# Optimization experiments

Hardware: AMD Instinct MI355X
Metric: run time of the kernel (lower is better)

The kernel has to match this reference:

```python
import jax, jax.numpy as jnp
import numpy as np

B, F, DEPTH = 8192, 256, 6

def entmax15(x):
    # exact 1.5-entmax along the last axis (sort-based algorithm)
    x = x / 2.0
    x = x - jnp.max(x, axis=-1, keepdims=True)
    xs = -jnp.sort(-x, axis=-1)                      # descending sort
    d = x.shape[-1]
    rho = jnp.arange(1, d + 1, dtype=x.dtype)
    mean = jnp.cumsum(xs, axis=-1) / rho
    mean_sq = jnp.cumsum(xs * xs, axis=-1) / rho
    ss = rho * (mean_sq - mean * mean)
    tau = mean - jnp.sqrt(jnp.clip((1.0 - ss) / rho, 0.0))
    support = jnp.sum((tau <= xs).astype(jnp.int32), axis=-1)
    tau_star = jnp.take_along_axis(tau, (support - 1)[..., None], axis=-1)
    return jnp.square(jnp.clip(x - tau_star, 0.0))

def _stump_level(x_in, fm, cp, lr):
    # x_in: [B,Fd]; fm: [n,Fd]; cp,lr: [n,Fd,2]. Vectorized over all n stumps of a level.
    mask = entmax15(fm)                                      # [n,Fd] feature gating
    w = jnp.array([1.0, 2.0], dtype=x_in.dtype)              # cutpoint-bin weights W
    z = entmax15(x_in[None, :, :, None] * w - cp[:, None])   # [n,B,Fd,2] binning
    out = jnp.einsum('nbfl,nfl,nf->nbl', z, lr, mask)        # leaf responses, masked sum over features
    # torch.cat of per-stump [B,2] along dim=1 -> [B, n*2]
    return jnp.transpose(out, (1, 0, 2)).reshape(x_in.shape[0], -1), mask

def _forward(x, params):
    tree_input = x
    masks = []
    out = None
    for fm, cp, lr in params:
        out, m = _stump_level(tree_input, fm, cp, lr)
        tree_input = jnp.concatenate([x, out], axis=1)
        masks.append(m)
    return out, masks

def setup_inputs() -> dict:
    key = jax.random.key(0)
    ks = jax.random.split(key, 1 + 3 * DEPTH)
    inp = {"x": jax.random.normal(ks[0], (B, F), dtype=jnp.float32)}
    for d in range(DEPTH):
        n = 2 ** d
        Fd = F + (2 ** d if d > 0 else 0)
        inp[f"fm{d}"] = jax.random.uniform(ks[1 + 3 * d], (n, Fd), dtype=jnp.float32)
        inp[f"cp{d}"] = jax.random.uniform(ks[2 + 3 * d], (n, Fd, 2), dtype=jnp.float32)
        inp[f"lr{d}"] = jax.random.uniform(ks[3 + 3 * d], (n, Fd, 2), dtype=jnp.float32)
    return inp

def reference(x, fm0, cp0, lr0, fm1, cp1, lr1, fm2, cp2, lr2, fm3, cp3, lr3, fm4, cp4, lr4, fm5, cp5, lr5):
    params = [(fm0, cp0, lr0), (fm1, cp1, lr1), (fm2, cp2, lr2),
              (fm3, cp3, lr3), (fm4, cp4, lr4), (fm5, cp5, lr5)]
    out, masks = _forward(x, params)  # dropout=0 -> identity
    return (out, *masks)
```

## Files before the change

### kernel.cpp

```cpp
#include <hip/hip_runtime.h>

#define B_SZ 8192


struct MaskArgs {
  const float* fm[6];
  const float* cp[6];
  const float* lr[6];
  float* out_masks;
  float4* cprm;
  int* cnt;
  float* cstf;
};

__device__ __forceinline__ float wave_max(float v) {
#pragma unroll
  for (int o = 32; o > 0; o >>= 1) v = fmaxf(v, __shfl_xor(v, o));
  return v;
}
__device__ __forceinline__ float wave_sum(float v) {
#pragma unroll
  for (int o = 32; o > 0; o >>= 1) v += __shfl_xor(v, o);
  return v;
}

__global__ __launch_bounds__(64) void ndt_masks(MaskArgs a) {
  const int maskOff[6] = {524288, 524544, 525060, 526100, 528212, 532564};
  const int prmOff[6]  = {0, 256, 772, 1812, 3924, 8276};
  const int cstOff[6]  = {0, 1, 3, 7, 15, 31};
  const int exBase[6]  = {0, 256, 258, 262, 270, 286};
  int bid = blockIdx.x, lane = threadIdx.x;
  int d = 0, s = bid, n = 1;
  while (s >= n) { s -= n; n <<= 1; ++d; }
  int Fd = 256 + ((d > 0) ? n : 0);

  const float* fm = a.fm[d] + (size_t)s * Fd;
  float y[5];
#pragma unroll
  for (int j = 0; j < 5; ++j) {
    int f = lane + 64 * j;
    y[j] = (f < Fd) ? fm[f] * 0.5f : -3.0e38f;
  }
  float m = fmaxf(fmaxf(fmaxf(y[0], y[1]), fmaxf(y[2], y[3])), y[4]);
  m = wave_max(m);
#pragma unroll
  for (int j = 0; j < 5; ++j) y[j] -= m;

  float lo = -1.f, hi = 0.f;
  for (int it = 0; it < 24; ++it) {
    float tau = 0.5f * (lo + hi);
    float ss = 0.f;
#pragma unroll
    for (int j = 0; j < 5; ++j) {
      float v = fmaxf(y[j] - tau, 0.f);
      ss = __builtin_fmaf(v, v, ss);
    }
    ss = wave_sum(ss);
    if (ss >= 1.f) lo = tau; else hi = tau;
  }
  float tau = 0.5f * (lo + hi);

  float* mo = a.out_masks + maskOff[d] + (size_t)s * Fd;
  const float* cp = a.cp[d] + (size_t)s * Fd * 2;
  const float* lr = a.lr[d] + (size_t)s * Fd * 2;
  float4* cpr = a.cprm + prmOff[d] + (size_t)s * Fd;
  int exB = exBase[d];
  float sum0 = 0.f, sum1 = 0.f;
  int base = 0;
#pragma unroll
  for (int j = 0; j < 5; ++j) {
    int f = lane + 64 * j;
    bool in = (f < Fd);
    float v = fmaxf(y[j] - tau, 0.f);
    float mk = v * v;
    float c10 = 0.f, ml0 = 0.f, ml1 = 0.f;
    if (in) {
      mo[f] = mk;
      float c0 = cp[2 * f], c1 = cp[2 * f + 1];
      ml0 = lr[2 * f] * mk;
      ml1 = lr[2 * f + 1] * mk;
      c10 = c1 - c0;
      sum0 += ml0;
      sum1 += ml1;
    }
    bool act = in && (v > 0.f);
    unsigned long long bm = __ballot(act);
    int pre = __popcll(bm & ((1ull << lane) - 1ull));
    if (act) {
      int fidx = (f < 256) ? f : (exB + f - 256);
      cpr[base + pre] =
          make_float4(c10, ml0 * 0.125f, ml1 * 0.125f, __int_as_float(fidx));
    }
    base += __popcll(bm);
  }
  sum0 = wave_sum(sum0);
  sum1 = wave_sum(sum1);
  if (lane == 0) {
    a.cstf[2 * (cstOff[d] + s)] = 0.5f * sum0;
    a.cstf[2 * (cstOff[d] + s) + 1] = 0.5f * sum1;
    a.cnt[cstOff[d] + s] = base;
  }
}

__device__ __forceinline__ float entpair(float c10, float xv) {
  float t = c10 - xv;
  float tc = __builtin_amdgcn_fmed3f(t, -2.f, 2.f);
  float u = __builtin_fmaf(tc, -tc, 8.0f);
  return tc * __builtin_amdgcn_sqrtf(u);
}

template <int N, int FD>
__device__ __forceinline__ void ndt_level(const float4* __restrict__ cp,
                                          const int* __restrict__ cN,
                                          const float* __restrict__ cs,
                                          int outRow, int g, int l,
                                          float* __restrict__ xls,
                                          float (*__restrict__ pbuf)[2][8]) {
  constexpr int SPG = 64 / N;
  int s = g / SPG, slice = g - s * SPG;
  int nc = cN[s];
  const float4* ps = cp + (size_t)s * FD;
  float a0 = 0.f, a1 = 0.f;
  int jlo = slice * nc / SPG, jhi = (slice + 1) * nc / SPG;
#pragma unroll 4
  for (int j = jlo; j < jhi; ++j) {
    float4 p = ps[j];
    int row = __float_as_int(p.w);
    float xv = xls[row * 9 + l];
    float e = entpair(p.x, xv);
    a0 = __builtin_fmaf(e, p.y, a0);
    a1 = __builtin_fmaf(-e, p.z, a1);
  }
  pbuf[g][0][l] = a0;
  pbuf[g][1][l] = a1;
  __syncthreads();
  for (int o = g; o < 2 * N; o += 64) {
    int s2 = o >> 1, par = o & 1;
    float v = cs[o];
#pragma unroll
    for (int k = 0; k < SPG; ++k) v += pbuf[s2 * SPG + k][par][l];
    xls[(outRow + o) * 9 + l] = v;
  }
  __syncthreads();
}

__global__ __launch_bounds__(512, 8) void ndt_all(const float* __restrict__ x,
                                                  const float4* __restrict__ cprm,
                                                  const int* __restrict__ cnt,
                                                  const float* __restrict__ cstf,
                                                  float* __restrict__ out) {
  __shared__ float xls[382 * 9];
  __shared__ float pbuf[64][2][8];
  int tid = threadIdx.x;
  int g = tid >> 3, l = tid & 7;
  int b0 = blockIdx.x * 8;
  {
    int c = tid >> 6, seg = tid & 63;
    float4 v = *(const float4*)(x + (size_t)(b0 + c) * 256 + seg * 4);
    int f = seg * 4;
    xls[(f + 0) * 9 + c] = v.x;
    xls[(f + 1) * 9 + c] = v.y;
    xls[(f + 2) * 9 + c] = v.z;
    xls[(f + 3) * 9 + c] = v.w;
  }
  __syncthreads();
  ndt_level<1, 256>(cprm, cnt, cstf, 256, g, l, xls, pbuf);
  ndt_level<2, 258>(cprm + 256, cnt + 1, cstf + 2, 258, g, l, xls, pbuf);
  ndt_level<4, 260>(cprm + 772, cnt + 3, cstf + 6, 262, g, l, xls, pbuf);
  ndt_level<8, 264>(cprm + 1812, cnt + 7, cstf + 14, 270, g, l, xls, pbuf);
  ndt_level<16, 272>(cprm + 3924, cnt + 15, cstf + 30, 286, g, l, xls, pbuf);
  ndt_level<32, 288>(cprm + 8276, cnt + 31, cstf + 62, 318, g, l, xls, pbuf);
  {
    int c = tid >> 6, o = tid & 63;
    out[(size_t)(b0 + c) * 64 + o] = xls[(318 + o) * 9 + c];
  }
}

extern "C" void kernel_launch(void* const* d_in, const int* in_sizes, int n_in,
                              void* d_out, int out_size, void* d_ws, size_t ws_size,
                              hipStream_t stream) {
  const float* x = (const float*)d_in[0];
  float* out = (float*)d_out;
  float* wsf = (float*)d_ws;

  float4* cprm = (float4*)(wsf + 2575872);
  float* cstf = wsf + 2645840;
  int* cnt = (int*)(wsf + 2645966);

  MaskArgs ma;
  for (int d = 0; d < 6; ++d) {
    ma.fm[d] = (const float*)d_in[1 + 3 * d];
    ma.cp[d] = (const float*)d_in[2 + 3 * d];
    ma.lr[d] = (const float*)d_in[3 + 3 * d];
  }
  ma.out_masks = out;
  ma.cprm = cprm;
  ma.cnt = cnt;
  ma.cstf = cstf;
  hipLaunchKernelGGL(ndt_masks, dim3(63), dim3(64), 0, stream, ma);

  hipLaunchKernelGGL(ndt_all, dim3(B_SZ / 8), dim3(512), 0, stream,
                     x, cprm, cnt, cstf, out);
}
```

Baseline: 44.18 us.

## Process 16 rows per block with paired-column reuse and XOR-swizzled LDS layout

Each block now handles 16 batch rows with 1024 threads, and each thread evaluates two batch columns per loaded cutpoint record. This halves the global float4 parameter loads per row and amortizes the loop overhead. The shared-memory x tile moves to a row stride of 18 with an XOR swizzle on column pairs, which allows float2 LDS reads and is meant to avoid bank conflicts. In exchange the block size doubles, so fewer blocks run (512) and more registers are needed per thread, which could lower occupancy.

```diff
diff --git a/kernel.cpp b/kernel.cpp
--- a/kernel.cpp
+++ b/kernel.cpp
@@ -109,59 +109,71 @@
   return tc * __builtin_amdgcn_sqrtf(u);
 }
 
+__device__ __forceinline__ int xidx(int row, int c) {
+  return row * 18 + 2 * ((c >> 1) ^ (row & 7)) + (c & 1);
+}
+
 template <int N, int FD>
 __device__ __forceinline__ void ndt_level(const float4* __restrict__ cp,
                                           const int* __restrict__ cN,
                                           const float* __restrict__ cs,
                                           int outRow, int g, int l,
                                           float* __restrict__ xls,
-                                          float (*__restrict__ pbuf)[2][8]) {
-  constexpr int SPG = 64 / N;
+                                          float (*__restrict__ pbuf)[2][16]) {
+  constexpr int SPG = 128 / N;
   int s = g / SPG, slice = g - s * SPG;
   int nc = cN[s];
   const float4* ps = cp + (size_t)s * FD;
-  float a0 = 0.f, a1 = 0.f;
+  float a00 = 0.f, a01 = 0.f, a10 = 0.f, a11 = 0.f;
   int jlo = slice * nc / SPG, jhi = (slice + 1) * nc / SPG;
 #pragma unroll 4
   for (int j = jlo; j < jhi; ++j) {
     float4 p = ps[j];
     int row = __float_as_int(p.w);
-    float xv = xls[row * 9 + l];
-    float e = entpair(p.x, xv);
-    a0 = __builtin_fmaf(e, p.y, a0);
-    a1 = __builtin_fmaf(-e, p.z, a1);
-  }
-  pbuf[g][0][l] = a0;
-  pbuf[g][1][l] = a1;
+    float2 xv = *(const float2*)&xls[row * 18 + 2 * (l ^ (row & 7))];
+    float e0 = entpair(p.x, xv.x);
+    float e1 = entpair(p.x, xv.y);
+    a00 = __builtin_fmaf(e0, p.y, a00);
+    a10 = __builtin_fmaf(-e0, p.z, a10);
+    a01 = __builtin_fmaf(e1, p.y, a01);
+    a11 = __builtin_fmaf(-e1, p.z, a11);
+  }
+  *(float2*)&pbuf[g][0][2 * l] = make_float2(a00, a01);
+  *(float2*)&pbuf[g][1][2 * l] = make_float2(a10, a11);
   __syncthreads();
-  for (int o = g; o < 2 * N; o += 64) {
+  for (int o = g; o < 2 * N; o += 128) {
     int s2 = o >> 1, par = o & 1;
-    float v = cs[o];
-#pragma unroll
-    for (int k = 0; k < SPG; ++k) v += pbuf[s2 * SPG + k][par][l];
-    xls[(outRow + o) * 9 + l] = v;
+    float v0 = cs[o], v1 = v0;
+#pragma unroll
+    for (int k = 0; k < SPG; ++k) {
+      float2 t = *(const float2*)&pbuf[s2 * SPG + k][par][2 * l];
+      v0 += t.x;
+      v1 += t.y;
+    }
+    int R = outRow + o;
+    *(float2*)&xls[R * 18 + 2 * (l ^ (R & 7))] = make_float2(v0, v1);
   }
   __syncthreads();
 }
 
-__global__ __launch_bounds__(512, 8) void ndt_all(const float* __restrict__ x,
-                                                  const float4* __restrict__ cprm,
-                                                  const int* __restrict__ cnt,
-                                                  const float* __restrict__ cstf,
-                                                  float* __restrict__ out) {
-  __shared__ float xls[382 * 9];
-  __shared__ float pbuf[64][2][8];
+__global__ __launch_bounds__(1024, 2) void ndt_all(const float* __restrict__ x,
+                                                   const float4* __restrict__ cprm,
+                                                   const int* __restrict__ cnt,
+                                                   const float* __restrict__ cstf,
+                                                   float* __restrict__ out) {
+  __shared__ float xls[382 * 18];
+  __shared__ float pbuf[128][2][16];
   int tid = threadIdx.x;
   int g = tid >> 3, l = tid & 7;
-  int b0 = blockIdx.x * 8;
+  int b0 = blockIdx.x * 16;
   {
     int c = tid >> 6, seg = tid & 63;
     float4 v = *(const float4*)(x + (size_t)(b0 + c) * 256 + seg * 4);
     int f = seg * 4;
-    xls[(f + 0) * 9 + c] = v.x;
-    xls[(f + 1) * 9 + c] = v.y;
-    xls[(f + 2) * 9 + c] = v.z;
-    xls[(f + 3) * 9 + c] = v.w;
+    xls[xidx(f + 0, c)] = v.x;
+    xls[xidx(f + 1, c)] = v.y;
+    xls[xidx(f + 2, c)] = v.z;
+    xls[xidx(f + 3, c)] = v.w;
   }
   __syncthreads();
   ndt_level<1, 256>(cprm, cnt, cstf, 256, g, l, xls, pbuf);
@@ -172,7 +184,7 @@
   ndt_level<32, 288>(cprm + 8276, cnt + 31, cstf + 62, 318, g, l, xls, pbuf);
   {
     int c = tid >> 6, o = tid & 63;
-    out[(size_t)(b0 + c) * 64 + o] = xls[(318 + o) * 9 + c];
+    out[(size_t)(b0 + c) * 64 + o] = xls[xidx(318 + o, c)];
   }
 }
 
@@ -199,6 +211,6 @@
   ma.cstf = cstf;
   hipLaunchKernelGGL(ndt_masks, dim3(63), dim3(64), 0, stream, ma);
 
-  hipLaunchKernelGGL(ndt_all, dim3(B_SZ / 8), dim3(512), 0, stream,
+  hipLaunchKernelGGL(ndt_all, dim3(B_SZ / 16), dim3(1024), 0, stream,
                      x, cprm, cnt, cstf, out);
 }
```

New measurement: 46.94 us. 6.2% more time.

## Remap stump work to whole wavefronts with shuffle reductions

Applied to the files above, without the earlier changes.

Reassigns the per-level work so that each 64-lane wavefront handles whole stumps (or wave-sized slices for small levels). Within a wave, lanes split as 8 active-feature slots by 8 batch rows, and partial sums are combined with cross-lane shuffles. For levels with 8 or more stumps this removes the shared-memory partial buffer and its extra barrier, and it shrinks pbuf. The aim is to cut LDS traffic and synchronisation and to balance the skewed per-thread slicing; occupancy bound is lowered from 8 to 4.

```diff
diff --git a/kernel.cpp b/kernel.cpp
--- a/kernel.cpp
+++ b/kernel.cpp
@@ -113,46 +113,91 @@
 __device__ __forceinline__ void ndt_level(const float4* __restrict__ cp,
                                           const int* __restrict__ cN,
                                           const float* __restrict__ cs,
-                                          int outRow, int g, int l,
+                                          int outRow, int w, int lane,
                                           float* __restrict__ xls,
                                           float (*__restrict__ pbuf)[2][8]) {
-  constexpr int SPG = 64 / N;
-  int s = g / SPG, slice = g - s * SPG;
-  int nc = cN[s];
-  const float4* ps = cp + (size_t)s * FD;
-  float a0 = 0.f, a1 = 0.f;
-  int jlo = slice * nc / SPG, jhi = (slice + 1) * nc / SPG;
-#pragma unroll 4
-  for (int j = jlo; j < jhi; ++j) {
-    float4 p = ps[j];
-    int row = __float_as_int(p.w);
-    float xv = xls[row * 9 + l];
-    float e = entpair(p.x, xv);
-    a0 = __builtin_fmaf(e, p.y, a0);
-    a1 = __builtin_fmaf(-e, p.z, a1);
-  }
-  pbuf[g][0][l] = a0;
-  pbuf[g][1][l] = a1;
-  __syncthreads();
-  for (int o = g; o < 2 * N; o += 64) {
-    int s2 = o >> 1, par = o & 1;
-    float v = cs[o];
-#pragma unroll
-    for (int k = 0; k < SPG; ++k) v += pbuf[s2 * SPG + k][par][l];
-    xls[(outRow + o) * 9 + l] = v;
-  }
-  __syncthreads();
-}
-
-__global__ __launch_bounds__(512, 8) void ndt_all(const float* __restrict__ x,
+  int e = lane >> 3, c = lane & 7;
+  if (N >= 8) {
+#pragma unroll
+    for (int k = 0; k < N / 8; ++k) {
+      int s = w + 8 * k;
+      int nc = cN[s];
+      const float4* ps = cp + (size_t)s * FD;
+      float a0 = 0.f, a1 = 0.f;
+      for (int j = 0; j < nc; j += 8) {
+        int jj = j + e;
+        if (jj < nc) {
+          float4 p = ps[jj];
+          int row = __float_as_int(p.w);
+          float xv = xls[row * 9 + c];
+          float ee = entpair(p.x, xv);
+          a0 = __builtin_fmaf(ee, p.y, a0);
+          a1 = __builtin_fmaf(-ee, p.z, a1);
+        }
+      }
+#pragma unroll
+      for (int m = 8; m < 64; m <<= 1) {
+        a0 += __shfl_xor(a0, m);
+        a1 += __shfl_xor(a1, m);
+      }
+      a0 += cs[2 * s];
+      a1 += cs[2 * s + 1];
+      if (lane < 8)
+        xls[(outRow + 2 * s) * 9 + c] = a0;
+      else if (lane < 16)
+        xls[(outRow + 2 * s + 1) * 9 + c] = a1;
+    }
+    __syncthreads();
+  } else {
+    constexpr int WPS = 8 / N;
+    int s = w / WPS, slice = w % WPS;
+    int nc = cN[s];
+    const float4* ps = cp + (size_t)s * FD;
+    int jlo = slice * nc / WPS, jhi = (slice + 1) * nc / WPS;
+    float a0 = 0.f, a1 = 0.f;
+    for (int j = jlo; j < jhi; j += 8) {
+      int jj = j + e;
+      if (jj < jhi) {
+        float4 p = ps[jj];
+        int row = __float_as_int(p.w);
+        float xv = xls[row * 9 + c];
+        float ee = entpair(p.x, xv);
+        a0 = __builtin_fmaf(ee, p.y, a0);
+        a1 = __builtin_fmaf(-ee, p.z, a1);
+      }
+    }
+#pragma unroll
+    for (int m = 8; m < 64; m <<= 1) {
+      a0 += __shfl_xor(a0, m);
+      a1 += __shfl_xor(a1, m);
+    }
+    if (lane < 8)
+      pbuf[w][0][c] = a0;
+    else if (lane < 16)
+      pbuf[w][1][c] = a1;
+    __syncthreads();
+    int tid = w * 64 + lane;
+    if (tid < 2 * N * 8) {
+      int o = tid >> 3, cc = tid & 7;
+      int s2 = o >> 1, par = o & 1;
+      float v = cs[o];
+#pragma unroll
+      for (int k = 0; k < WPS; ++k) v += pbuf[s2 * WPS + k][par][cc];
+      xls[(outRow + o) * 9 + cc] = v;
+    }
+    __syncthreads();
+  }
+}
+
+__global__ __launch_bounds__(512, 4) void ndt_all(const float* __restrict__ x,
                                                   const float4* __restrict__ cprm,
                                                   const int* __restrict__ cnt,
                                                   const float* __restrict__ cstf,
                                                   float* __restrict__ out) {
   __shared__ float xls[382 * 9];
-  __shared__ float pbuf[64][2][8];
+  __shared__ float pbuf[8][2][8];
   int tid = threadIdx.x;
-  int g = tid >> 3, l = tid & 7;
+  int w = tid >> 6, lane = tid & 63;
   int b0 = blockIdx.x * 8;
   {
     int c = tid >> 6, seg = tid & 63;
@@ -164,12 +209,12 @@
     xls[(f + 3) * 9 + c] = v.w;
   }
   __syncthreads();
-  ndt_level<1, 256>(cprm, cnt, cstf, 256, g, l, xls, pbuf);
-  ndt_level<2, 258>(cprm + 256, cnt + 1, cstf + 2, 258, g, l, xls, pbuf);
-  ndt_level<4, 260>(cprm + 772, cnt + 3, cstf + 6, 262, g, l, xls, pbuf);
-  ndt_level<8, 264>(cprm + 1812, cnt + 7, cstf + 14, 270, g, l, xls, pbuf);
-  ndt_level<16, 272>(cprm + 3924, cnt + 15, cstf + 30, 286, g, l, xls, pbuf);
-  ndt_level<32, 288>(cprm + 8276, cnt + 31, cstf + 62, 318, g, l, xls, pbuf);
+  ndt_level<1, 256>(cprm, cnt, cstf, 256, w, lane, xls, pbuf);
+  ndt_level<2, 258>(cprm + 256, cnt + 1, cstf + 2, 258, w, lane, xls, pbuf);
+  ndt_level<4, 260>(cprm + 772, cnt + 3, cstf + 6, 262, w, lane, xls, pbuf);
+  ndt_level<8, 264>(cprm + 1812, cnt + 7, cstf + 14, 270, w, lane, xls, pbuf);
+  ndt_level<16, 272>(cprm + 3924, cnt + 15, cstf + 30, 286, w, lane, xls, pbuf);
+  ndt_level<32, 288>(cprm + 8276, cnt + 31, cstf + 62, 318, w, lane, xls, pbuf);
   {
     int c = tid >> 6, o = tid & 63;
     out[(size_t)(b0 + c) * 64 + o] = xls[(318 + o) * 9 + c];
```

Result: slower. 58.61 us (+32.7%).

## Process sixteen batch rows per block, reusing each stump parameter load twice

Applied to the files above, without the earlier changes.

Each thread now handles two batch columns per stump parameter, so every float4 parameter load from global memory feeds two entmax pair evaluations. Each block covers 16 rows instead of 8, which halves the grid and the number of parameter streams across blocks. Shared memory is restrided (stride 17) and the reduction and output stores are reworked, with float2 output writes. The cost is more shared memory and registers per block, a lower launch-bounds occupancy hint, and fewer blocks (512) to spread across the GPU.

```diff
diff --git a/kernel.cpp b/kernel.cpp
--- a/kernel.cpp
+++ b/kernel.cpp
@@ -1,6 +1,7 @@
 #include <hip/hip_runtime.h>
 
 #define B_SZ 8192
+#define XST 17
 
 
 struct MaskArgs {
@@ -114,65 +115,72 @@
                                           const int* __restrict__ cN,
                                           const float* __restrict__ cs,
                                           int outRow, int g, int l,
-                                          float* __restrict__ xls,
-                                          float (*__restrict__ pbuf)[2][8]) {
+                                          float* __restrict__ pbuf,
+                                          float* __restrict__ xls) {
   constexpr int SPG = 64 / N;
   int s = g / SPG, slice = g - s * SPG;
   int nc = cN[s];
   const float4* ps = cp + (size_t)s * FD;
-  float a0 = 0.f, a1 = 0.f;
+  float a00 = 0.f, a10 = 0.f, a01 = 0.f, a11 = 0.f;
   int jlo = slice * nc / SPG, jhi = (slice + 1) * nc / SPG;
 #pragma unroll 4
   for (int j = jlo; j < jhi; ++j) {
     float4 p = ps[j];
     int row = __float_as_int(p.w);
-    float xv = xls[row * 9 + l];
-    float e = entpair(p.x, xv);
-    a0 = __builtin_fmaf(e, p.y, a0);
-    a1 = __builtin_fmaf(-e, p.z, a1);
-  }
-  pbuf[g][0][l] = a0;
-  pbuf[g][1][l] = a1;
+    float xv0 = xls[row * XST + l];
+    float xv1 = xls[row * XST + l + 8];
+    float e0 = entpair(p.x, xv0);
+    float e1 = entpair(p.x, xv1);
+    a00 = __builtin_fmaf(e0, p.y, a00);
+    a10 = __builtin_fmaf(-e0, p.z, a10);
+    a01 = __builtin_fmaf(e1, p.y, a01);
+    a11 = __builtin_fmaf(-e1, p.z, a11);
+  }
+  pbuf[g * 32 + l] = a00;
+  pbuf[g * 32 + l + 8] = a01;
+  pbuf[g * 32 + 16 + l] = a10;
+  pbuf[g * 32 + 16 + l + 8] = a11;
   __syncthreads();
-  for (int o = g; o < 2 * N; o += 64) {
+  int tid = g * 8 + l;
+  for (int t = tid; t < 2 * N * 16; t += 512) {
+    int o = t >> 4, cc = t & 15;
     int s2 = o >> 1, par = o & 1;
     float v = cs[o];
 #pragma unroll
-    for (int k = 0; k < SPG; ++k) v += pbuf[s2 * SPG + k][par][l];
-    xls[(outRow + o) * 9 + l] = v;
+    for (int k = 0; k < SPG; ++k)
+      v += pbuf[(s2 * SPG + k) * 32 + par * 16 + cc];
+    xls[(outRow + o) * XST + cc] = v;
   }
   __syncthreads();
 }
 
-__global__ __launch_bounds__(512, 8) void ndt_all(const float* __restrict__ x,
+__global__ __launch_bounds__(512, 4) void ndt_all(const float* __restrict__ x,
                                                   const float4* __restrict__ cprm,
                                                   const int* __restrict__ cnt,
                                                   const float* __restrict__ cstf,
                                                   float* __restrict__ out) {
-  __shared__ float xls[382 * 9];
-  __shared__ float pbuf[64][2][8];
+  __shared__ float xls[382 * XST];
+  __shared__ float pbuf[64 * 32];
   int tid = threadIdx.x;
   int g = tid >> 3, l = tid & 7;
-  int b0 = blockIdx.x * 8;
+  int b0 = blockIdx.x * 16;
   {
-    int c = tid >> 6, seg = tid & 63;
-    float4 v = *(const float4*)(x + (size_t)(b0 + c) * 256 + seg * 4);
-    int f = seg * 4;
-    xls[(f + 0) * 9 + c] = v.x;
-    xls[(f + 1) * 9 + c] = v.y;
-    xls[(f + 2) * 9 + c] = v.z;
-    xls[(f + 3) * 9 + c] = v.w;
+    int c = tid >> 5, seg = tid & 31;
+    const float* xp = x + (size_t)(b0 + c) * 256 + seg;
+#pragma unroll
+    for (int j = 0; j < 8; ++j) xls[(seg + 32 * j) * XST + c] = xp[32 * j];
   }
   __syncthreads();
-  ndt_level<1, 256>(cprm, cnt, cstf, 256, g, l, xls, pbuf);
-  ndt_level<2, 258>(cprm + 256, cnt + 1, cstf + 2, 258, g, l, xls, pbuf);
-  ndt_level<4, 260>(cprm + 772, cnt + 3, cstf + 6, 262, g, l, xls, pbuf);
-  ndt_level<8, 264>(cprm + 1812, cnt + 7, cstf + 14, 270, g, l, xls, pbuf);
-  ndt_level<16, 272>(cprm + 3924, cnt + 15, cstf + 30, 286, g, l, xls, pbuf);
-  ndt_level<32, 288>(cprm + 8276, cnt + 31, cstf + 62, 318, g, l, xls, pbuf);
+  ndt_level<1, 256>(cprm, cnt, cstf, 256, g, l, pbuf, xls);
+  ndt_level<2, 258>(cprm + 256, cnt + 1, cstf + 2, 258, g, l, pbuf, xls);
+  ndt_level<4, 260>(cprm + 772, cnt + 3, cstf + 6, 262, g, l, pbuf, xls);
+  ndt_level<8, 264>(cprm + 1812, cnt + 7, cstf + 14, 270, g, l, pbuf, xls);
+  ndt_level<16, 272>(cprm + 3924, cnt + 15, cstf + 30, 286, g, l, pbuf, xls);
+  ndt_level<32, 288>(cprm + 8276, cnt + 31, cstf + 62, 318, g, l, pbuf, xls);
   {
-    int c = tid >> 6, o = tid & 63;
-    out[(size_t)(b0 + c) * 64 + o] = xls[(318 + o) * 9 + c];
+    int c = tid >> 5, oo = (tid & 31) * 2;
+    float2 v = make_float2(xls[(318 + oo) * XST + c], xls[(319 + oo) * XST + c]);
+    *(float2*)(out + (size_t)(b0 + c) * 64 + oo) = v;
   }
 }
 
@@ -199,6 +207,6 @@
   ma.cstf = cstf;
   hipLaunchKernelGGL(ndt_masks, dim3(63), dim3(64), 0, stream, ma);
 
-  hipLaunchKernelGGL(ndt_all, dim3(B_SZ / 8), dim3(512), 0, stream,
+  hipLaunchKernelGGL(ndt_all, dim3(B_SZ / 16), dim3(512), 0, stream,
                      x, cprm, cnt, cstf, out);
 }
```

After: 37.65 us, median of 2. 14.8% less time.
